# Kernel optimization log

Hardware: AMD Instinct MI355X
Metric: run time of the kernel (lower is better)

The kernel has to match this reference:

```python
import jax, jax.numpy as jnp
import numpy as np

DIM, DEPTH, HEADS, MLP = 1024, 6, 16, 4096
HEAD_DIM = DIM // HEADS
SCALE = DIM ** -0.5  # NOTE: original uses full dim, not head_dim
EPS = 1e-5


def _layernorm(x, g, b):
    m = jnp.mean(x, axis=-1, keepdims=True)
    v = jnp.mean((x - m) ** 2, axis=-1, keepdims=True)
    return (x - m) * jax.lax.rsqrt(v + EPS) * g + b


def setup_inputs() -> dict:
    key = jax.random.key(0)
    ks = jax.random.split(key, 12)
    d = DEPTH
    s_qkv = (DIM * 3) ** -0.5  # ~kaiming-ish scale, values only need to be plausible
    inp = {
        "x": jax.random.normal(ks[0], (2, 2048, DIM), dtype=jnp.float32),
        "Wqkv": jax.random.normal(ks[1], (d, DIM, 3 * DIM), dtype=jnp.float32) * s_qkv,
        "Wout": jax.random.normal(ks[2], (d, DIM, DIM), dtype=jnp.float32) * (DIM ** -0.5),
        "bout": jnp.zeros((d, DIM), dtype=jnp.float32),
        "ln1_g": jnp.ones((d, DIM), dtype=jnp.float32),
        "ln1_b": jnp.zeros((d, DIM), dtype=jnp.float32),
        "ln2_g": jnp.ones((d, DIM), dtype=jnp.float32),
        "ln2_b": jnp.zeros((d, DIM), dtype=jnp.float32),
        "W1": jax.random.normal(ks[3], (d, DIM, MLP), dtype=jnp.float32) * (DIM ** -0.5),
        "b1": jnp.zeros((d, MLP), dtype=jnp.float32),
        "W2": jax.random.normal(ks[4], (d, MLP, DIM), dtype=jnp.float32) * (MLP ** -0.5),
        "b2": jnp.zeros((d, DIM), dtype=jnp.float32),
    }
    return inp


def _transformer(x, Wqkv, Wout, bout, ln1_g, ln1_b, ln2_g, ln2_b, W1, b1, W2, b2):
    b, n, _ = x.shape

    def layer(h, p):
        wqkv, wout, bo, g1, bb1, g2, bb2, w1, bf1, w2, bf2 = p
        # --- attention block (Residual(PreNorm(SelfAttention))) ---
        y = _layernorm(h, g1, bb1)
        qkv = y @ wqkv                                   # [b, n, 3*dim]
        qkv = qkv.reshape(b, n, 3, HEADS, HEAD_DIM)
        q, k, v = [jnp.transpose(qkv[:, :, i], (0, 2, 1, 3)) for i in range(3)]  # [b,h,n,d]
        dots = jnp.einsum("bhid,bhjd->bhij", q, k) * SCALE
        attn = jax.nn.softmax(dots, axis=-1)
        o = jnp.einsum("bhij,bhjd->bhid", attn, v)       # [b,h,n,d]
        o = jnp.transpose(o, (0, 2, 1, 3)).reshape(b, n, DIM)
        h = h + (o @ wout + bo)
        # --- FFN block (Residual(PreNorm(FeedForward))) ---
        y = _layernorm(h, g2, bb2)
        y = jax.nn.gelu(y @ w1 + bf1, approximate=False) @ w2 + bf2
        return h + y, None

    params = (Wqkv, Wout, bout, ln1_g, ln1_b, ln2_g, ln2_b, W1, b1, W2, b2)
    out, _ = jax.lax.scan(layer, x, params)
    return out


def reference(x, Wqkv, Wout, bout, ln1_g, ln1_b, ln2_g, ln2_b, W1, b1, W2, b2):
    return _transformer(x, Wqkv, Wout, bout, ln1_g, ln1_b, ln2_g, ln2_b, W1, b1, W2, b2)
```

## Files before the change

### kernel.cpp

```cpp
#include <hip/hip_runtime.h>
#include <hip/hip_bf16.h>
#include <math.h>

typedef __attribute__((__ext_vector_type__(8))) __bf16 bf16x8;
typedef __attribute__((__ext_vector_type__(4))) float f32x4;

#define DIMQ 1024
#define SEQ 2048
#define NTOK 4096
#define HEADS 16
#define HD 64
#define MLPD 4096
#define DEPTH 6

__device__ __forceinline__ void gl_lds16(const __hip_bfloat16* g, __hip_bfloat16* l) {
  __builtin_amdgcn_global_load_lds((const __attribute__((address_space(1))) void*)(g),
                                   (__attribute__((address_space(3))) void*)(l), 16, 0, 0);
}

__global__ __launch_bounds__(256) void ln_kernel(const float* __restrict__ h,
                                                 const float* __restrict__ g,
                                                 const float* __restrict__ bta,
                                                 __hip_bfloat16* __restrict__ y) {
  int row = blockIdx.x;
  int t = threadIdx.x;
  const float4* src = (const float4*)(h + (size_t)row * DIMQ);
  float4 xv = src[t];
  float s = xv.x + xv.y + xv.z + xv.w;
  float ss = xv.x * xv.x + xv.y * xv.y + xv.z * xv.z + xv.w * xv.w;
#pragma unroll
  for (int off = 32; off > 0; off >>= 1) {
    s += __shfl_xor(s, off);
    ss += __shfl_xor(ss, off);
  }
  __shared__ float red[8];
  int wid = t >> 6;
  if ((t & 63) == 0) { red[wid] = s; red[4 + wid] = ss; }
  __syncthreads();
  s = red[0] + red[1] + red[2] + red[3];
  ss = red[4] + red[5] + red[6] + red[7];
  float mean = s * (1.0f / DIMQ);
  float var = ss * (1.0f / DIMQ) - mean * mean;
  float rstd = rsqrtf(var + 1e-5f);
  float4 gv = ((const float4*)g)[t];
  float4 bv = ((const float4*)bta)[t];
  __hip_bfloat16* dst = y + (size_t)row * DIMQ + t * 4;
  dst[0] = __float2bfloat16((xv.x - mean) * rstd * gv.x + bv.x);
  dst[1] = __float2bfloat16((xv.y - mean) * rstd * gv.y + bv.y);
  dst[2] = __float2bfloat16((xv.z - mean) * rstd * gv.z + bv.z);
  dst[3] = __float2bfloat16((xv.w - mean) * rstd * gv.w + bv.w);
}

__global__ __launch_bounds__(256) void transpose_cast(const float* __restrict__ in,
                                                      __hip_bfloat16* __restrict__ out,
                                                      int K, int N) {
  __shared__ float t[32][33];
  int n0 = blockIdx.x * 32, k0 = blockIdx.y * 32;
  int tx = threadIdx.x, ty = threadIdx.y;
#pragma unroll
  for (int i = 0; i < 32; i += 8)
    t[ty + i][tx] = in[(size_t)(k0 + ty + i) * N + n0 + tx];
  __syncthreads();
#pragma unroll
  for (int i = 0; i < 32; i += 8)
    out[(size_t)(n0 + ty + i) * K + k0 + tx] = __float2bfloat16(t[tx][ty + i]);
}

__global__ __launch_bounds__(256) void vtrans(const __hip_bfloat16* __restrict__ qkvb,
                                              __hip_bfloat16* __restrict__ vT) {
  __shared__ __hip_bfloat16 t[32][33];
  int n0 = blockIdx.x * 32, d0 = blockIdx.y * 32, bh = blockIdx.z;
  int tx = threadIdx.x, ty = threadIdx.y;
#pragma unroll
  for (int i = 0; i < 32; i += 8)
    t[ty + i][tx] = qkvb[((size_t)(64 + bh) * SEQ + n0 + ty + i) * HD + d0 + tx];
  __syncthreads();
#pragma unroll
  for (int i = 0; i < 32; i += 8)
    vT[((size_t)bh * HD + d0 + ty + i) * SEQ + n0 + tx] = t[tx][ty + i];
}

template <int EPI, int SPLITK>
__global__ __launch_bounds__(256)
void gemm_kernel(const __hip_bfloat16* __restrict__ A, const __hip_bfloat16* __restrict__ BT,
                 const float* __restrict__ bias, void* __restrict__ outp,
                 int M, int N, int K) {
  __shared__ __hip_bfloat16 As[128][64];
  __shared__ __hip_bfloat16 Bs[128][64];
  int tid = threadIdx.x;
  int m0 = blockIdx.y * 128, n0 = blockIdx.x * 128;
  int lane = tid & 63, wid = tid >> 6;
  int l16 = lane & 15, quad = lane >> 4;
  int wm = (wid >> 1) * 64, wn = (wid & 1) * 64;
  int srsub = lane >> 3;
  int sg = (lane & 7) ^ srsub;
  int Kc = K / SPLITK;
  int k0 = blockIdx.z * Kc;
  f32x4 acc[4][4] = {};
  for (int kt = 0; kt < Kc; kt += 64) {
    __syncthreads();
#pragma unroll
    for (int s = 0; s < 4; ++s) {
      int r0 = (wid * 4 + s) * 8;
      gl_lds16(A + (size_t)(m0 + r0 + srsub) * K + k0 + kt + sg * 8, &As[r0][0]);
      gl_lds16(BT + (size_t)(n0 + r0 + srsub) * K + k0 + kt + sg * 8, &Bs[r0][0]);
    }
    __syncthreads();
#pragma unroll
    for (int ks = 0; ks < 2; ++ks) {
      bf16x8 af[4], bfr[4];
      int p = (ks * 4 + quad) ^ (l16 & 7);
#pragma unroll
      for (int i = 0; i < 4; ++i) af[i] = *(const bf16x8*)&As[wm + i * 16 + l16][p * 8];
#pragma unroll
      for (int j = 0; j < 4; ++j) bfr[j] = *(const bf16x8*)&Bs[wn + j * 16 + l16][p * 8];
#pragma unroll
      for (int i = 0; i < 4; ++i)
#pragma unroll
        for (int j = 0; j < 4; ++j)
          acc[i][j] = __builtin_amdgcn_mfma_f32_16x16x32_bf16(af[i], bfr[j], acc[i][j], 0, 0, 0);
    }
  }
#pragma unroll
  for (int j = 0; j < 4; ++j) {
    int col = n0 + wn + j * 16 + l16;
    float bv = (EPI == 3) ? 0.0f : bias[col];
#pragma unroll
    for (int i = 0; i < 4; ++i) {
#pragma unroll
      for (int r = 0; r < 4; ++r) {
        int row = m0 + wm + i * 16 + quad * 4 + r;
        float v = acc[i][j][r];
        if (EPI == 1) {
          v += bv;
          v = 0.5f * v * (1.0f + erff(v * 0.70710678118654752f));
          ((__hip_bfloat16*)outp)[(size_t)row * N + col] = __float2bfloat16(v);
        } else if (EPI == 2) {
          float add = v + ((SPLITK == 1 || blockIdx.z == 0) ? bv : 0.0f);
          unsafeAtomicAdd(&((float*)outp)[(size_t)row * N + col], add);
        } else {
          int which = col >> 10;
          int head = (col >> 6) & 15;
          int d = col & 63;
          size_t dst = (((size_t)which * 32 + (row >> 11) * 16 + head) * SEQ + (row & 2047)) * HD + d;
          ((__hip_bfloat16*)outp)[dst] = __float2bfloat16(v);
        }
      }
    }
  }
}

__global__ __launch_bounds__(256)
void attn_kernel(const __hip_bfloat16* __restrict__ qkvb, const __hip_bfloat16* __restrict__ vT,
                 __hip_bfloat16* __restrict__ o) {
  __shared__ __hip_bfloat16 Ks[64][64];
  __shared__ __hip_bfloat16 Vs[64][64];
  __shared__ __hip_bfloat16 Ps[4][16][68];
  int bh = blockIdx.y;
  int b = bh >> 4;
  int tid = threadIdx.x;
  int wid = tid >> 6, lane = tid & 63;
  int l16 = lane & 15, quad = lane >> 4;
  int qrow = blockIdx.x * 64 + wid * 16 + l16;
  const __hip_bfloat16* qp = qkvb + ((size_t)bh * SEQ + qrow) * HD;
  bf16x8 qf0 = *(const bf16x8*)(qp + quad * 8);
  bf16x8 qf1 = *(const bf16x8*)(qp + 32 + quad * 8);
  f32x4 oacc[4] = {};
  float lsum[4] = {0.0f, 0.0f, 0.0f, 0.0f};
  int srsub = lane >> 3;
  int sg = (lane & 7) ^ srsub;
  const __hip_bfloat16* kbase = qkvb + (size_t)(32 + bh) * SEQ * HD;
  const __hip_bfloat16* vbase = vT + (size_t)bh * HD * SEQ;
  const float c1 = 0.045084220027780106f;
  for (int kb = 0; kb < SEQ; kb += 64) {
    __syncthreads();
    {
      int r0 = wid * 16, r1 = wid * 16 + 8;
      gl_lds16(kbase + (size_t)(kb + r0 + srsub) * HD + sg * 8, &Ks[r0][0]);
      gl_lds16(kbase + (size_t)(kb + r1 + srsub) * HD + sg * 8, &Ks[r1][0]);
      gl_lds16(vbase + (size_t)(r0 + srsub) * SEQ + kb + sg * 8, &Vs[r0][0]);
      gl_lds16(vbase + (size_t)(r1 + srsub) * SEQ + kb + sg * 8, &Vs[r1][0]);
    }
    __syncthreads();
    f32x4 sc[4];
    int p0 = quad ^ (l16 & 7);
    int p1 = (4 + quad) ^ (l16 & 7);
#pragma unroll
    for (int c = 0; c < 4; ++c) {
      int r = c * 16 + l16;
      bf16x8 k0 = *(const bf16x8*)&Ks[r][p0 * 8];
      bf16x8 k1 = *(const bf16x8*)&Ks[r][p1 * 8];
      f32x4 z = {};
      z = __builtin_amdgcn_mfma_f32_16x16x32_bf16(qf0, k0, z, 0, 0, 0);
      z = __builtin_amdgcn_mfma_f32_16x16x32_bf16(qf1, k1, z, 0, 0, 0);
      sc[c] = z;
    }
#pragma unroll
    for (int r = 0; r < 4; ++r) {
      float psum = 0.0f;
#pragma unroll
      for (int c = 0; c < 4; ++c) {
        float p = exp2f(sc[c][r] * c1);
        psum += p;
        Ps[wid][quad * 4 + r][c * 16 + l16] = __float2bfloat16(p);
      }
      lsum[r] += psum;
    }
    asm volatile("s_waitcnt lgkmcnt(0)" ::: "memory");
    bf16x8 pf0 = *(const bf16x8*)&Ps[wid][l16][quad * 8];
    bf16x8 pf1 = *(const bf16x8*)&Ps[wid][l16][32 + quad * 8];
#pragma unroll
    for (int f = 0; f < 4; ++f) {
      int r = f * 16 + l16;
      bf16x8 v0 = *(const bf16x8*)&Vs[r][p0 * 8];
      bf16x8 v1 = *(const bf16x8*)&Vs[r][p1 * 8];
      oacc[f] = __builtin_amdgcn_mfma_f32_16x16x32_bf16(pf0, v0, oacc[f], 0, 0, 0);
      oacc[f] = __builtin_amdgcn_mfma_f32_16x16x32_bf16(pf1, v1, oacc[f], 0, 0, 0);
    }
  }
#pragma unroll
  for (int r = 0; r < 4; ++r) {
#pragma unroll
    for (int off = 1; off < 16; off <<= 1) lsum[r] += __shfl_xor(lsum[r], off);
  }
  int h = bh & 15;
  int orow = b * SEQ + blockIdx.x * 64 + wid * 16 + quad * 4;
#pragma unroll
  for (int r = 0; r < 4; ++r) {
    float inv = 1.0f / lsum[r];
#pragma unroll
    for (int f = 0; f < 4; ++f) {
      o[(size_t)(orow + r) * DIMQ + h * HD + f * 16 + l16] = __float2bfloat16(oacc[f][r] * inv);
    }
  }
}

extern "C" void kernel_launch(void* const* d_in, const int* in_sizes, int n_in,
                              void* d_out, int out_size, void* d_ws, size_t ws_size,
                              hipStream_t stream) {
  const float* x = (const float*)d_in[0];
  const float* Wqkv = (const float*)d_in[1];
  const float* Wout = (const float*)d_in[2];
  const float* bout = (const float*)d_in[3];
  const float* ln1g = (const float*)d_in[4];
  const float* ln1b = (const float*)d_in[5];
  const float* ln2g = (const float*)d_in[6];
  const float* ln2b = (const float*)d_in[7];
  const float* W1 = (const float*)d_in[8];
  const float* b1 = (const float*)d_in[9];
  const float* W2 = (const float*)d_in[10];
  const float* b2 = (const float*)d_in[11];
  float* h = (float*)d_out;

  char* ws = (char*)d_ws;
  __hip_bfloat16* wqkvT = (__hip_bfloat16*)ws; ws += (size_t)3072 * 1024 * 2;
  __hip_bfloat16* woutT = (__hip_bfloat16*)ws; ws += (size_t)1024 * 1024 * 2;
  __hip_bfloat16* w1T = (__hip_bfloat16*)ws;   ws += (size_t)4096 * 1024 * 2;
  __hip_bfloat16* w2T = (__hip_bfloat16*)ws;   ws += (size_t)1024 * 4096 * 2;
  __hip_bfloat16* ybuf = (__hip_bfloat16*)ws;  ws += (size_t)NTOK * 1024 * 2;
  __hip_bfloat16* qkvb = (__hip_bfloat16*)ws;  ws += (size_t)NTOK * 3072 * 2;
  __hip_bfloat16* vTb = (__hip_bfloat16*)ws;   ws += (size_t)32 * HD * SEQ * 2;
  __hip_bfloat16* obuf = (__hip_bfloat16*)ws;  ws += (size_t)NTOK * 1024 * 2;
  __hip_bfloat16* actb = (__hip_bfloat16*)ws;  ws += (size_t)NTOK * MLPD * 2;

  hipMemcpyAsync(h, x, (size_t)out_size * sizeof(float), hipMemcpyDeviceToDevice, stream);

  dim3 tb(32, 8);
  for (int l = 0; l < DEPTH; ++l) {
    transpose_cast<<<dim3(3072 / 32, 1024 / 32), tb, 0, stream>>>(
        Wqkv + (size_t)l * 1024 * 3072, wqkvT, 1024, 3072);
    transpose_cast<<<dim3(1024 / 32, 1024 / 32), tb, 0, stream>>>(
        Wout + (size_t)l * 1024 * 1024, woutT, 1024, 1024);
    transpose_cast<<<dim3(4096 / 32, 1024 / 32), tb, 0, stream>>>(
        W1 + (size_t)l * 1024 * 4096, w1T, 1024, 4096);
    transpose_cast<<<dim3(1024 / 32, 4096 / 32), tb, 0, stream>>>(
        W2 + (size_t)l * 4096 * 1024, w2T, 4096, 1024);

    ln_kernel<<<NTOK, 256, 0, stream>>>(h, ln1g + l * 1024, ln1b + l * 1024, ybuf);
    gemm_kernel<3, 1><<<dim3(3072 / 128, NTOK / 128, 1), 256, 0, stream>>>(
        ybuf, wqkvT, nullptr, qkvb, NTOK, 3072, 1024);
    vtrans<<<dim3(SEQ / 32, 2, 32), tb, 0, stream>>>(qkvb, vTb);
    attn_kernel<<<dim3(SEQ / 64, 32), 256, 0, stream>>>(qkvb, vTb, obuf);
    gemm_kernel<2, 2><<<dim3(1024 / 128, NTOK / 128, 2), 256, 0, stream>>>(
        obuf, woutT, bout + l * 1024, h, NTOK, 1024, 1024);

    ln_kernel<<<NTOK, 256, 0, stream>>>(h, ln2g + l * 1024, ln2b + l * 1024, ybuf);
    gemm_kernel<1, 1><<<dim3(4096 / 128, NTOK / 128, 1), 256, 0, stream>>>(
        ybuf, w1T, b1 + l * 4096, actb, NTOK, 4096, 1024);
    gemm_kernel<2, 4><<<dim3(1024 / 128, NTOK / 128, 4), 256, 0, stream>>>(
        actb, w2T, b2 + l * 1024, h, NTOK, 1024, 4096);
  }
}
```

Before: 2.136 ms.

## Replace split-K atomic GEMMs with 128x64 residual GEMM and XCD-aware tile mapping

Drops split-K with float atomics for the output and FFN-down projections. They are replaced by a 128x64-tile GEMM that accumulates the full K per block and adds the residual and bias directly into h. All GEMMs now use a 1D grid that maps consecutive block IDs to N-tile groups per XCD, to improve L2 locality of the weight tiles. The trade-off is a longer serial K loop per block in exchange for no atomic traffic, and a different wave count per launch.

Measured after the change: 1.988 ms. -6.9%, faster.

```diff
diff --git a/kernel.cpp b/kernel.cpp
--- a/kernel.cpp
+++ b/kernel.cpp
@@ -80,30 +80,31 @@
     vT[((size_t)bh * HD + d0 + ty + i) * SEQ + n0 + tx] = t[tx][ty + i];
 }
 
-template <int EPI, int SPLITK>
+template <int EPI>
 __global__ __launch_bounds__(256)
-void gemm_kernel(const __hip_bfloat16* __restrict__ A, const __hip_bfloat16* __restrict__ BT,
-                 const float* __restrict__ bias, void* __restrict__ outp,
-                 int M, int N, int K) {
+void gemm128(const __hip_bfloat16* __restrict__ A, const __hip_bfloat16* __restrict__ BT,
+             const float* __restrict__ bias, void* __restrict__ outp,
+             int M, int N, int K, int gpx) {
   __shared__ __hip_bfloat16 As[128][64];
   __shared__ __hip_bfloat16 Bs[128][64];
+  int bid = blockIdx.x;
+  int xcd = bid & 7, jb = bid >> 3;
+  int nt = xcd * gpx + (jb % gpx), mt = jb / gpx;
+  int m0 = mt * 128, n0 = nt * 128;
   int tid = threadIdx.x;
-  int m0 = blockIdx.y * 128, n0 = blockIdx.x * 128;
   int lane = tid & 63, wid = tid >> 6;
   int l16 = lane & 15, quad = lane >> 4;
   int wm = (wid >> 1) * 64, wn = (wid & 1) * 64;
   int srsub = lane >> 3;
   int sg = (lane & 7) ^ srsub;
-  int Kc = K / SPLITK;
-  int k0 = blockIdx.z * Kc;
   f32x4 acc[4][4] = {};
-  for (int kt = 0; kt < Kc; kt += 64) {
+  for (int kt = 0; kt < K; kt += 64) {
     __syncthreads();
 #pragma unroll
     for (int s = 0; s < 4; ++s) {
       int r0 = (wid * 4 + s) * 8;
-      gl_lds16(A + (size_t)(m0 + r0 + srsub) * K + k0 + kt + sg * 8, &As[r0][0]);
-      gl_lds16(BT + (size_t)(n0 + r0 + srsub) * K + k0 + kt + sg * 8, &Bs[r0][0]);
+      gl_lds16(A + (size_t)(m0 + r0 + srsub) * K + kt + sg * 8, &As[r0][0]);
+      gl_lds16(BT + (size_t)(n0 + r0 + srsub) * K + kt + sg * 8, &Bs[r0][0]);
     }
     __syncthreads();
 #pragma unroll
@@ -135,9 +136,6 @@
           v += bv;
           v = 0.5f * v * (1.0f + erff(v * 0.70710678118654752f));
           ((__hip_bfloat16*)outp)[(size_t)row * N + col] = __float2bfloat16(v);
-        } else if (EPI == 2) {
-          float add = v + ((SPLITK == 1 || blockIdx.z == 0) ? bv : 0.0f);
-          unsafeAtomicAdd(&((float*)outp)[(size_t)row * N + col], add);
         } else {
           int which = col >> 10;
           int head = (col >> 6) & 15;
@@ -145,6 +143,67 @@
           size_t dst = (((size_t)which * 32 + (row >> 11) * 16 + head) * SEQ + (row & 2047)) * HD + d;
           ((__hip_bfloat16*)outp)[dst] = __float2bfloat16(v);
         }
+      }
+    }
+  }
+}
+
+__global__ __launch_bounds__(256, 5)
+void gemm64_res(const __hip_bfloat16* __restrict__ A, const __hip_bfloat16* __restrict__ BT,
+                const float* __restrict__ bias, float* __restrict__ h,
+                int M, int N, int K, int gpx) {
+  __shared__ __hip_bfloat16 As[128][64];
+  __shared__ __hip_bfloat16 Bs[64][64];
+  int bid = blockIdx.x;
+  int xcd = bid & 7, jb = bid >> 3;
+  int nt = xcd * gpx + (jb % gpx), mt = jb / gpx;
+  int m0 = mt * 128, n0 = nt * 64;
+  int tid = threadIdx.x;
+  int lane = tid & 63, wid = tid >> 6;
+  int l16 = lane & 15, quad = lane >> 4;
+  int wm = (wid >> 1) * 64, wn = (wid & 1) * 32;
+  int srsub = lane >> 3;
+  int sg = (lane & 7) ^ srsub;
+  f32x4 acc[4][2] = {};
+  for (int kt = 0; kt < K; kt += 64) {
+    __syncthreads();
+#pragma unroll
+    for (int s = 0; s < 4; ++s) {
+      int r0 = (wid * 4 + s) * 8;
+      gl_lds16(A + (size_t)(m0 + r0 + srsub) * K + kt + sg * 8, &As[r0][0]);
+    }
+#pragma unroll
+    for (int s = 0; s < 2; ++s) {
+      int r0 = (wid * 2 + s) * 8;
+      gl_lds16(BT + (size_t)(n0 + r0 + srsub) * K + kt + sg * 8, &Bs[r0][0]);
+    }
+    __syncthreads();
+#pragma unroll
+    for (int ks = 0; ks < 2; ++ks) {
+      bf16x8 af[4], bfr[2];
+      int p = (ks * 4 + quad) ^ (l16 & 7);
+#pragma unroll
+      for (int i = 0; i < 4; ++i) af[i] = *(const bf16x8*)&As[wm + i * 16 + l16][p * 8];
+#pragma unroll
+      for (int j = 0; j < 2; ++j) bfr[j] = *(const bf16x8*)&Bs[wn + j * 16 + l16][p * 8];
+#pragma unroll
+      for (int i = 0; i < 4; ++i)
+#pragma unroll
+        for (int j = 0; j < 2; ++j)
+          acc[i][j] = __builtin_amdgcn_mfma_f32_16x16x32_bf16(af[i], bfr[j], acc[i][j], 0, 0, 0);
+    }
+  }
+#pragma unroll
+  for (int j = 0; j < 2; ++j) {
+    int col = n0 + wn + j * 16 + l16;
+    float bv = bias[col];
+#pragma unroll
+    for (int i = 0; i < 4; ++i) {
+#pragma unroll
+      for (int r = 0; r < 4; ++r) {
+        int row = m0 + wm + i * 16 + quad * 4 + r;
+        size_t idx = (size_t)row * N + col;
+        h[idx] = h[idx] + acc[i][j][r] + bv;
       }
     }
   }
@@ -277,17 +336,13 @@
         W2 + (size_t)l * 4096 * 1024, w2T, 4096, 1024);
 
     ln_kernel<<<NTOK, 256, 0, stream>>>(h, ln1g + l * 1024, ln1b + l * 1024, ybuf);
-    gemm_kernel<3, 1><<<dim3(3072 / 128, NTOK / 128, 1), 256, 0, stream>>>(
-        ybuf, wqkvT, nullptr, qkvb, NTOK, 3072, 1024);
+    gemm128<3><<<768, 256, 0, stream>>>(ybuf, wqkvT, nullptr, qkvb, NTOK, 3072, 1024, 3);
     vtrans<<<dim3(SEQ / 32, 2, 32), tb, 0, stream>>>(qkvb, vTb);
     attn_kernel<<<dim3(SEQ / 64, 32), 256, 0, stream>>>(qkvb, vTb, obuf);
-    gemm_kernel<2, 2><<<dim3(1024 / 128, NTOK / 128, 2), 256, 0, stream>>>(
-        obuf, woutT, bout + l * 1024, h, NTOK, 1024, 1024);
+    gemm64_res<<<512, 256, 0, stream>>>(obuf, woutT, bout + l * 1024, h, NTOK, 1024, 1024, 2);
 
     ln_kernel<<<NTOK, 256, 0, stream>>>(h, ln2g + l * 1024, ln2b + l * 1024, ybuf);
-    gemm_kernel<1, 1><<<dim3(4096 / 128, NTOK / 128, 1), 256, 0, stream>>>(
-        ybuf, w1T, b1 + l * 4096, actb, NTOK, 4096, 1024);
-    gemm_kernel<2, 4><<<dim3(1024 / 128, NTOK / 128, 4), 256, 0, stream>>>(
-        actb, w2T, b2 + l * 1024, h, NTOK, 1024, 4096);
-  }
-}
+    gemm128<1><<<1024, 256, 0, stream>>>(ybuf, w1T, b1 + l * 4096, actb, NTOK, 4096, 1024, 4);
+    gemm64_res<<<512, 256, 0, stream>>>(actb, w2T, b2 + l * 1024, h, NTOK, 1024, 4096, 2);
+  }
+}
```
